# Kernel optimization log

Hardware: AMD Instinct MI355X
Metric: run time of the kernel (lower is better)

Reference implementation:

```python
import jax, jax.numpy as jnp
import numpy as np

B, C, N, T = 8, 128, 512, 64


def setup_inputs() -> dict:
    key = jax.random.key(0)
    ks = jax.random.split(key, 16)
    s = 0.05  # small init scale to keep softmax well-conditioned
    return {
        "x": jax.random.normal(ks[0], (B, C, N, T), jnp.float32),
        "W_w": jax.random.normal(ks[1], (C, C), jnp.float32) * s,
        "W_b": jax.random.normal(ks[2], (C,), jnp.float32) * s,
        "conv_w": jax.random.normal(ks[3], (C, C), jnp.float32) * s,
        "conv_b": jax.random.normal(ks[4], (C,), jnp.float32) * s,
        "theta": jax.random.normal(ks[5], (C, C), jnp.float32) * s,
        "memory": jax.random.normal(ks[6], (N, C), jnp.float32) * s,
        "a_vec": jax.random.uniform(ks[7], (2 * C, 1), jnp.float32) * s,
        "cw": jax.random.normal(ks[8], (N, N), jnp.float32) * s,
        "cwa": jax.random.normal(ks[9], (N, N), jnp.float32) * s,
        "fc_w": jax.random.normal(ks[10], (1, 2), jnp.float32) * s,
        "fc_b": jax.random.normal(ks[11], (1,), jnp.float32) * s,
        "emb": jax.random.normal(ks[12], (1, C, N, 1), jnp.float32),
        "cheb": jax.random.normal(ks[13], (1, N, N), jnp.float32),  # loaded but unused, as in torch forward
    }


def reference(x, W_w, W_b, conv_w, conv_b, theta, memory, a_vec, cw, cwa, fc_w, fc_b, emb, cheb):
    c = x.shape[1]
    skip = x
    # 1x1 conv W: [B,C,N,T] -> [B,C,N,T]
    xw = jnp.einsum('bcnt,dc->bdnt', x, W_w) + W_b[None, :, None, None]
    # Adaptive_Spectral_Block (dropout = identity in eval)
    x_in = jnp.transpose(xw, (0, 3, 2, 1))          # [B,T,N,C]
    h = x_in.sum(axis=1)                             # [B,N,C]
    Wh1 = h @ a_vec[:c]                              # [B,N,1]
    Wh2 = h @ a_vec[c:]                              # [B,N,1]
    e = Wh1 + jnp.transpose(Wh2, (0, 2, 1))          # [B,N,N]
    adj_w = e * cw
    scale = 1.0 / jnp.sqrt(jnp.asarray(c, x.dtype))
    adj1 = jax.nn.softmax(jax.nn.relu(jnp.einsum('btnc,mc->bnm', x_in, memory) * scale), axis=-1)
    adj2 = jax.nn.softmax(jax.nn.relu(jnp.einsum('bnc,bmc->bnm', h, h) * scale), axis=-1)
    # fc: Linear(2,1) over stacked adjacencies, then squeeze
    adj_f = jnp.stack([adj1, adj2], axis=-1) @ fc_w[0] + fc_b[0]   # [B,N,N]
    adj_w = adj_w + adj_f * cwa
    adj_w = jax.nn.softmax(adj_w, axis=-1)
    # top-k (k = int(0.8*N)) + scatter mask
    n = adj_w.shape[-1]
    k = int(n * 0.8)
    _, idx = jax.lax.top_k(adj_w, k)                 # [B,N,k]
    bi = jnp.arange(adj_w.shape[0])[:, None, None]
    ni = jnp.arange(n)[None, :, None]
    mask = jnp.zeros_like(adj_w).at[bi, ni, idx].set(1.0)
    adj = adj_w * mask
    # diffusion aggregation + per-channel Theta transform (single head)
    xh = jnp.einsum('bcnt,bnm->bcmt', xw, adj)
    xh = jnp.einsum('bcnt,cd->bdnt', xh, theta)
    # 1x1 conv over concatenated heads (head=1)
    out = jnp.einsum('bcnt,dc->bdnt', xh, conv_w) + conv_b[None, :, None, None]
    return out * emb + skip
```

## Files before the change

### kernel.cpp

```cpp
#include <hip/hip_runtime.h>
#include <cstdint>
#include <cstddef>

#define KSEL 409u
typedef unsigned short ushort;
typedef short s16x8 __attribute__((ext_vector_type(8)));
typedef float f32x4 __attribute__((ext_vector_type(4)));

union FragU { uint4 u; s16x8 v; };

__device__ __forceinline__ ushort f2bf(float f) {
  union { float f; unsigned u; } x; x.f = f;
  unsigned u = x.u;
  return (ushort)((u + 0x7fffu + ((u >> 16) & 1u)) >> 16);
}

#define OFF_YW     0u
#define OFF_XS     16777216u
#define OFF_H      17301504u
#define OFF_HT     17825792u
#define OFF_WH1    18350080u
#define OFF_WH2    18354176u
#define OFF_ADJ    18358272u
#define OFF_ADJT   20455424u
#define OFF_MEMT   21504000u
#define OFF_WWT    21569536u
#define OFF_M      21585920u
#define OFF_PB16   21602304u
#define OFF_PBIAS  21610496u

__global__ __launch_bounds__(256) void k_pre1(
    const float* __restrict__ memory, const float* __restrict__ W_w,
    const float* __restrict__ conv_w, const float* __restrict__ theta,
    float* __restrict__ memT, float* __restrict__ WwT, float* __restrict__ Mm) {
  int idx = blockIdx.x * 256 + threadIdx.x;
  if (idx < 65536) {
    int c = idx >> 9, m = idx & 511;
    memT[idx] = memory[m * 128 + c];
  } else if (idx < 81920) {
    int i2 = idx - 65536;
    int cp = i2 >> 7, c = i2 & 127;
    WwT[i2] = W_w[c * 128 + cp];
  } else if (idx < 98304) {
    int i3 = idx - 81920;
    int d = i3 >> 7, e = i3 & 127;
    float s = 0.f;
    for (int c = 0; c < 128; ++c) s += conv_w[d * 128 + c] * theta[e * 128 + c];
    Mm[i3] = s;
  }
}

__global__ __launch_bounds__(256) void k_pre2(
    const float* __restrict__ Mm, const float* __restrict__ W_w,
    const float* __restrict__ W_b, ushort* __restrict__ Pb, float* __restrict__ pbias) {
  int idx = blockIdx.x * 256 + threadIdx.x;
  if (idx < 16384) {
    int d = idx >> 7, c = idx & 127;
    float s = 0.f;
    for (int e = 0; e < 128; ++e) s += Mm[d * 128 + e] * W_w[e * 128 + c];
    Pb[d * 128 + c] = f2bf(s);
    if (idx < 128) {
      float s2 = 0.f;
      for (int e = 0; e < 128; ++e) s2 += Mm[idx * 128 + e] * W_b[e];
      pbias[idx] = s2;
    }
  }
}

#define XB_STRIDE 138
#define PB_STRIDE 136
#define OUT_STRIDE 68
__global__ __launch_bounds__(256, 4) void k_yw(
    const float* __restrict__ x, const ushort* __restrict__ Pbg,
    const float* __restrict__ pbias, ushort* __restrict__ ywg, float* __restrict__ Xs) {
  __shared__ __align__(16) ushort pbl[128 * PB_STRIDE];
  __shared__ __align__(16) ushort xbuf[64 * XB_STRIDE];
  __shared__ float pbias_sh[128];
  int bid = blockIdx.x;
  int b = bid >> 9, n = bid & 511;
  int tid = threadIdx.x;
  int lane = tid & 63, w = tid >> 6;
  int quad = lane >> 4, lx = lane & 15;

  for (int k = 0; k < 8; ++k) {
    int flat8 = tid + 256 * k;
    int d = flat8 >> 4, cseg = flat8 & 15;
    uint4 v = *(const uint4*)(Pbg + d * 128 + cseg * 8);
    *(uint4*)&pbl[d * PB_STRIDE + cseg * 8] = v;
  }
  if (tid < 128) pbias_sh[tid] = pbias[tid];

  const float* xbase = x + (size_t)b * 4194304 + (size_t)n * 64;
  for (int k = 0; k < 8; ++k) {
    int c = (tid >> 4) + 16 * k;
    int t0 = (tid & 15) * 4;
    float4 v = *(const float4*)(xbase + (size_t)c * 32768 + t0);
    xbuf[(t0 + 0) * XB_STRIDE + c] = f2bf(v.x);
    xbuf[(t0 + 1) * XB_STRIDE + c] = f2bf(v.y);
    xbuf[(t0 + 2) * XB_STRIDE + c] = f2bf(v.z);
    xbuf[(t0 + 3) * XB_STRIDE + c] = f2bf(v.w);
    float s = v.x + v.y + v.z + v.w;
    s += __shfl_xor(s, 1, 64);
    s += __shfl_xor(s, 2, 64);
    s += __shfl_xor(s, 4, 64);
    s += __shfl_xor(s, 8, 64);
    if ((tid & 15) == 0) Xs[((size_t)(b * 512 + n)) * 128 + c] = s;
  }
  __syncthreads();

  f32x4 acc[8];
  #pragma unroll
  for (int i = 0; i < 8; ++i) acc[i] = (f32x4){0.f, 0.f, 0.f, 0.f};
  int tp = lx + 16 * w;
  const unsigned* xb32 = (const unsigned*)xbuf;
  #pragma unroll
  for (int kc = 0; kc < 4; ++kc) {
    FragU bf;
    int bbase = tp * (XB_STRIDE / 2) + kc * 16 + quad * 4;
    bf.u.x = xb32[bbase + 0];
    bf.u.y = xb32[bbase + 1];
    bf.u.z = xb32[bbase + 2];
    bf.u.w = xb32[bbase + 3];
    #pragma unroll
    for (int dt = 0; dt < 8; ++dt) {
      FragU af;
      af.u = *(const uint4*)&pbl[(16 * dt + lx) * PB_STRIDE + kc * 32 + quad * 8];
      acc[dt] = __builtin_amdgcn_mfma_f32_16x16x32_bf16(af.v, bf.v, acc[dt], 0, 0, 0);
    }
  }
  __syncthreads();
  #pragma unroll
  for (int dt = 0; dt < 8; ++dt)
    #pragma unroll
    for (int r = 0; r < 4; ++r) {
      int d = 16 * dt + quad * 4 + r;
      xbuf[d * OUT_STRIDE + tp] = f2bf(acc[dt][r] + pbias_sh[d]);
    }
  __syncthreads();
  for (int k = 0; k < 4; ++k) {
    int flat8 = tid + 256 * k;
    int d = flat8 >> 3, t0 = (flat8 & 7) * 8;
    ushort4 u0 = *(const ushort4*)&xbuf[d * OUT_STRIDE + t0];
    ushort4 u1 = *(const ushort4*)&xbuf[d * OUT_STRIDE + t0 + 4];
    ushort* dst = ywg + (((size_t)(b * 128 + d)) * 512 + n) * 64 + t0;
    uint4 pk;
    pk.x = (unsigned)u0.x | ((unsigned)u0.y << 16);
    pk.y = (unsigned)u0.z | ((unsigned)u0.w << 16);
    pk.z = (unsigned)u1.x | ((unsigned)u1.y << 16);
    pk.w = (unsigned)u1.z | ((unsigned)u1.w << 16);
    *(uint4*)dst = pk;
  }
}

__global__ __launch_bounds__(256) void k_h(
    const float* __restrict__ Xs, const float* __restrict__ WwT,
    const float* __restrict__ W_b, const float* __restrict__ a_vec,
    float* __restrict__ h, float* __restrict__ hT,
    float* __restrict__ Wh1, float* __restrict__ Wh2) {
  __shared__ float wt[64 * 128];
  __shared__ float xs[8 * 128];
  __shared__ float hr[8 * 128];
  __shared__ float av[256];
  int tid = threadIdx.x;
  int row0 = blockIdx.x * 8;
  for (int i = tid; i < 1024; i += 256) xs[i] = Xs[(size_t)row0 * 128 + i];
  av[tid] = a_vec[tid];
  int c = tid & 127;
  int r0 = tid >> 7;
  float wb = W_b[c] * 64.f;
  float acc[4];
  #pragma unroll
  for (int k = 0; k < 4; ++k) acc[k] = wb;
  for (int ch = 0; ch < 2; ++ch) {
    int cp0 = ch * 64;
    __syncthreads();
    for (int i = tid; i < 8192; i += 256) wt[i] = WwT[(size_t)cp0 * 128 + i];
    __syncthreads();
    for (int cpl = 0; cpl < 64; ++cpl) {
      float w = wt[cpl * 128 + c];
      #pragma unroll
      for (int k = 0; k < 4; ++k) acc[k] += xs[(r0 + 2 * k) * 128 + cp0 + cpl] * w;
    }
  }
  #pragma unroll
  for (int k = 0; k < 4; ++k) {
    int r = r0 + 2 * k;
    int rowg = row0 + r;
    int b = rowg >> 9, n = rowg & 511;
    h[(size_t)rowg * 128 + c] = acc[k];
    hT[((size_t)(b * 128 + c)) * 512 + n] = acc[k];
    hr[r * 128 + c] = acc[k];
  }
  __syncthreads();
  if (tid < 8) {
    float w1 = 0.f, w2 = 0.f;
    for (int cc = 0; cc < 128; ++cc) {
      float hv = hr[tid * 128 + cc];
      w1 += hv * av[cc];
      w2 += hv * av[128 + cc];
    }
    Wh1[row0 + tid] = w1;
    Wh2[row0 + tid] = w2;
  }
}

__device__ __forceinline__ void reduce_rows4(float v[4], float* sred, int tid, bool domax) {
  int lane = tid & 63, wid = tid >> 6;
  #pragma unroll
  for (int off = 32; off > 0; off >>= 1) {
    #pragma unroll
    for (int r = 0; r < 4; ++r) {
      float o = __shfl_down(v[r], off, 64);
      v[r] = domax ? fmaxf(v[r], o) : (v[r] + o);
    }
  }
  if (lane == 0) {
    #pragma unroll
    for (int r = 0; r < 4; ++r) sred[r * 4 + wid] = v[r];
  }
  __syncthreads();
  #pragma unroll
  for (int r = 0; r < 4; ++r) {
    float a0 = sred[r * 4 + 0], a1 = sred[r * 4 + 1];
    float a2 = sred[r * 4 + 2], a3 = sred[r * 4 + 3];
    v[r] = domax ? fmaxf(fmaxf(a0, a1), fmaxf(a2, a3)) : (a0 + a1 + a2 + a3);
  }
  __syncthreads();
}

__device__ __forceinline__ void softmax_rows4(float v[4][2], float* sred, int tid) {
  float mx[4];
  #pragma unroll
  for (int r = 0; r < 4; ++r) mx[r] = fmaxf(v[r][0], v[r][1]);
  reduce_rows4(mx, sred, tid, true);
  float sm[4];
  #pragma unroll
  for (int r = 0; r < 4; ++r) {
    v[r][0] = expf(v[r][0] - mx[r]);
    v[r][1] = expf(v[r][1] - mx[r]);
    sm[r] = v[r][0] + v[r][1];
  }
  reduce_rows4(sm, sred, tid, false);
  #pragma unroll
  for (int r = 0; r < 4; ++r) {
    float inv = 1.f / sm[r];
    v[r][0] *= inv;
    v[r][1] *= inv;
  }
}

__global__ __launch_bounds__(256) void k_adj(
    const float* __restrict__ h, const float* __restrict__ hT,
    const float* __restrict__ memT, const float* __restrict__ Wh1,
    const float* __restrict__ Wh2, const float* __restrict__ cw,
    const float* __restrict__ cwa, const float* __restrict__ fc_w,
    const float* __restrict__ fc_b, float* __restrict__ adj) {
  __shared__ float hn[4 * 128];
  __shared__ float sred[16];
  __shared__ unsigned scnt[124];
  int tid = threadIdx.x;
  int b = blockIdx.x >> 7;
  int n0 = (blockIdx.x & 127) * 4;
  for (int i = tid; i < 512; i += 256) hn[i] = h[((size_t)(b * 512 + n0)) * 128 + i];
  for (int i = tid; i < 124; i += 256) scnt[i] = 0u;
  __syncthreads();
  int m0 = tid, m1 = tid + 256;
  float d1[4][2] = {}, d2[4][2] = {};
  for (int c = 0; c < 128; ++c) {
    float mv0 = memT[c * 512 + m0];
    float mv1 = memT[c * 512 + m1];
    const float* hTr = hT + ((size_t)(b * 128 + c)) * 512;
    float hv0 = hTr[m0];
    float hv1 = hTr[m1];
    #pragma unroll
    for (int r = 0; r < 4; ++r) {
      float hc = hn[r * 128 + c];
      d1[r][0] += hc * mv0; d1[r][1] += hc * mv1;
      d2[r][0] += hc * hv0; d2[r][1] += hc * hv1;
    }
  }
  const float scale = 0.08838834764831845f;
  float l1[4][2], l2[4][2];
  #pragma unroll
  for (int r = 0; r < 4; ++r)
    #pragma unroll
    for (int s = 0; s < 2; ++s) {
      l1[r][s] = fmaxf(d1[r][s] * scale, 0.f);
      l2[r][s] = fmaxf(d2[r][s] * scale, 0.f);
    }
  softmax_rows4(l1, sred, tid);
  softmax_rows4(l2, sred, tid);
  float f0 = fc_w[0], f1 = fc_w[1], fb = fc_b[0];
  float wh2v[2] = {Wh2[b * 512 + m0], Wh2[b * 512 + m1]};
  float aw[4][2];
  #pragma unroll
  for (int r = 0; r < 4; ++r) {
    int n = n0 + r;
    float wh1v = Wh1[b * 512 + n];
    #pragma unroll
    for (int s = 0; s < 2; ++s) {
      int m = s ? m1 : m0;
      float e = wh1v + wh2v[s];
      float adjf = f0 * l1[r][s] + f1 * l2[r][s] + fb;
      aw[r][s] = e * cw[n * 512 + m] + adjf * cwa[n * 512 + m];
    }
  }
  softmax_rows4(aw, sred, tid);
  unsigned ua[4][2];
  #pragma unroll
  for (int r = 0; r < 4; ++r) {
    ua[r][0] = __float_as_uint(aw[r][0]);
    ua[r][1] = __float_as_uint(aw[r][1]);
  }
  unsigned cand[4] = {0u, 0u, 0u, 0u};
  int lane = tid & 63;
  for (int bit = 30; bit >= 0; --bit) {
    unsigned msk = 1u << bit;
    #pragma unroll
    for (int r = 0; r < 4; ++r) {
      unsigned tst = cand[r] | msk;
      unsigned long long b0 = __ballot(ua[r][0] >= tst);
      unsigned long long b1 = __ballot(ua[r][1] >= tst);
      if (lane == 0)
        atomicAdd(&scnt[bit * 4 + r], (unsigned)(__popcll(b0) + __popcll(b1)));
    }
    __syncthreads();
    #pragma unroll
    for (int r = 0; r < 4; ++r)
      if (scnt[bit * 4 + r] >= KSEL) cand[r] |= msk;
  }
  #pragma unroll
  for (int r = 0; r < 4; ++r) {
    size_t base = ((size_t)(b * 512 + n0 + r)) * 512;
    adj[base + m0] = (ua[r][0] >= cand[r]) ? aw[r][0] : 0.f;
    adj[base + m1] = (ua[r][1] >= cand[r]) ? aw[r][1] : 0.f;
  }
}

__global__ __launch_bounds__(256) void k_adjT(
    const float* __restrict__ adj, ushort* __restrict__ adjT) {
  __shared__ float tile[32][33];
  int gid = blockIdx.x;
  int b = gid >> 8;
  int tn = (gid & 255) >> 4, tm = gid & 15;
  int n0 = tn * 32, m0 = tm * 32;
  int tid = threadIdx.x;
  int nl = tid >> 3, ms = (tid & 7) * 4;
  float4 v = *(const float4*)(adj + (size_t)b * 262144 + (size_t)(n0 + nl) * 512 + m0 + ms);
  tile[nl][ms + 0] = v.x; tile[nl][ms + 1] = v.y;
  tile[nl][ms + 2] = v.z; tile[nl][ms + 3] = v.w;
  __syncthreads();
  int ml = tid >> 3, ns = (tid & 7) * 4;
  ushort4 o;
  o.x = f2bf(tile[ns + 0][ml]);
  o.y = f2bf(tile[ns + 1][ml]);
  o.z = f2bf(tile[ns + 2][ml]);
  o.w = f2bf(tile[ns + 3][ml]);
  *(ushort4*)(adjT + (size_t)b * 262144 + (size_t)(m0 + ml) * 512 + n0 + ns) = o;
}

#define AJ_STRIDE 40
#define YB_STRIDE 82
__global__ __launch_bounds__(512, 4) void k_out(
    const ushort* __restrict__ ywg, const ushort* __restrict__ adjT,
    const float* __restrict__ conv_b, const float* __restrict__ emb,
    const float* __restrict__ x, float* __restrict__ out) {
  __shared__ __align__(16) ushort adjt[512 * AJ_STRIDE];
  __shared__ __align__(16) ushort ywb[64 * YB_STRIDE];
  __shared__ float semb[512];
  int gid = blockIdx.x;
  int b = gid >> 7, d = gid & 127;
  int tid = threadIdx.x;
  int lane = tid & 63, w = tid >> 6;
  int quad = lane >> 4, lx = lane & 15;
  for (int i = tid; i < 512; i += 512) semb[i] = emb[d * 512 + i];
  float cb = conv_b[d];
  const ushort* adjTb = adjT + (size_t)b * 262144;
  const ushort* ywbase = ywg + ((size_t)(b * 128 + d)) * 32768;
  f32x4 acc[4][4];
  #pragma unroll
  for (int i = 0; i < 4; ++i)
    #pragma unroll
    for (int j = 0; j < 4; ++j) acc[i][j] = (f32x4){0.f, 0.f, 0.f, 0.f};
  const unsigned* ywb32 = (const unsigned*)ywb;

  for (int nc = 0; nc < 16; ++nc) {
    if (nc) __syncthreads();
    {
      int ml = tid >> 2, seg = tid & 3;
      #pragma unroll
      for (int kk = 0; kk < 4; ++kk) {
        int m = ml + 128 * kk;
        uint4 v = *(const uint4*)(adjTb + (size_t)m * 512 + nc * 32 + seg * 8);
        *(uint4*)&adjt[m * AJ_STRIDE + seg * 8] = v;
      }
    }
    {
      int t = tid & 63, nl = tid >> 6;
      #pragma unroll
      for (int kk = 0; kk < 4; ++kk) {
        int n_loc = nl + 8 * kk;
        ushort v = ywbase[(size_t)(nc * 32 + n_loc) * 64 + t];
        ywb[t * YB_STRIDE + n_loc] = v;
      }
    }
    __syncthreads();
    FragU bf[4];
    #pragma unroll
    for (int tt = 0; tt < 4; ++tt) {
      int t = lx + 16 * tt;
      int bb = t * (YB_STRIDE / 2) + quad * 4;
      bf[tt].u.x = ywb32[bb + 0];
      bf[tt].u.y = ywb32[bb + 1];
      bf[tt].u.z = ywb32[bb + 2];
      bf[tt].u.w = ywb32[bb + 3];
    }
    #pragma unroll
    for (int mt = 0; mt < 4; ++mt) {
      int m = 64 * w + 16 * mt + lx;
      FragU af;
      af.u = *(const uint4*)&adjt[m * AJ_STRIDE + quad * 8];
      #pragma unroll
      for (int tt = 0; tt < 4; ++tt)
        acc[mt][tt] = __builtin_amdgcn_mfma_f32_16x16x32_bf16(af.v, bf[tt].v, acc[mt][tt], 0, 0, 0);
    }
  }
  size_t obase = ((size_t)(b * 128 + d)) * 32768;
  #pragma unroll
  for (int mt = 0; mt < 4; ++mt) {
    #pragma unroll
    for (int r = 0; r < 4; ++r) {
      int m = 64 * w + 16 * mt + quad * 4 + r;
      float em = semb[m];
      #pragma unroll
      for (int tt = 0; tt < 4; ++tt) {
        int t = lx + 16 * tt;
        size_t idx = obase + (size_t)m * 64 + t;
        out[idx] = (acc[mt][tt][r] + cb) * em + x[idx];
      }
    }
  }
}

extern "C" void kernel_launch(void* const* d_in, const int* in_sizes, int n_in,
                              void* d_out, int out_size, void* d_ws, size_t ws_size,
                              hipStream_t stream) {
  const float* x      = (const float*)d_in[0];
  const float* W_w    = (const float*)d_in[1];
  const float* W_b    = (const float*)d_in[2];
  const float* conv_w = (const float*)d_in[3];
  const float* conv_b = (const float*)d_in[4];
  const float* theta  = (const float*)d_in[5];
  const float* memory = (const float*)d_in[6];
  const float* a_vec  = (const float*)d_in[7];
  const float* cw     = (const float*)d_in[8];
  const float* cwa    = (const float*)d_in[9];
  const float* fc_w   = (const float*)d_in[10];
  const float* fc_b   = (const float*)d_in[11];
  const float* emb    = (const float*)d_in[12];
  float* out = (float*)d_out;
  float* ws = (float*)d_ws;
  ushort* ywbf  = (ushort*)(ws + OFF_YW);
  float* Xs     = ws + OFF_XS;
  float* h      = ws + OFF_H;
  float* hT     = ws + OFF_HT;
  float* Wh1    = ws + OFF_WH1;
  float* Wh2    = ws + OFF_WH2;
  float* adj    = ws + OFF_ADJ;
  ushort* adjT  = (ushort*)(ws + OFF_ADJT);
  float* memT   = ws + OFF_MEMT;
  float* WwT    = ws + OFF_WWT;
  float* Mm     = ws + OFF_M;
  ushort* Pb    = (ushort*)(ws + OFF_PB16);
  float* pbias  = ws + OFF_PBIAS;

  hipLaunchKernelGGL(k_pre1, dim3(384), dim3(256), 0, stream,
                     memory, W_w, conv_w, theta, memT, WwT, Mm);
  hipLaunchKernelGGL(k_pre2, dim3(64), dim3(256), 0, stream, Mm, W_w, W_b, Pb, pbias);
  hipLaunchKernelGGL(k_yw, dim3(4096), dim3(256), 0, stream, x, Pb, pbias, ywbf, Xs);
  hipLaunchKernelGGL(k_h, dim3(512), dim3(256), 0, stream,
                     Xs, WwT, W_b, a_vec, h, hT, Wh1, Wh2);
  hipLaunchKernelGGL(k_adj, dim3(1024), dim3(256), 0, stream,
                     h, hT, memT, Wh1, Wh2, cw, cwa, fc_w, fc_b, adj);
  hipLaunchKernelGGL(k_adjT, dim3(2048), dim3(256), 0, stream, adj, adjT);
  hipLaunchKernelGGL(k_out, dim3(1024), dim3(512), 0, stream,
                     ywbf, adjT, conv_b, emb, x, out);
}
```

Measured before the change: 438.0 us.

## Fuse adjacency transpose into k_adj and prefetch k_out tiles into registers

k_adj now writes the masked adjacency directly as transposed bf16, so the fp32 adj buffer and the separate k_adjT transpose kernel are removed. This saves one launch and an fp32 round trip through memory. The cost is scattered 2-byte strided stores from k_adj. Separately, k_out loads the next chunk of adjT and yw into registers while it runs MFMAs on the current chunk, overlapping global latency with compute at the expense of more registers.

Result: no change. 432.0 us (-1.4%).

```diff
diff --git a/kernel.cpp b/kernel.cpp
--- a/kernel.cpp
+++ b/kernel.cpp
@@ -21,13 +21,12 @@
 #define OFF_HT     17825792u
 #define OFF_WH1    18350080u
 #define OFF_WH2    18354176u
-#define OFF_ADJ    18358272u
-#define OFF_ADJT   20455424u
-#define OFF_MEMT   21504000u
-#define OFF_WWT    21569536u
-#define OFF_M      21585920u
-#define OFF_PB16   21602304u
-#define OFF_PBIAS  21610496u
+#define OFF_ADJT   18358272u
+#define OFF_MEMT   19406848u
+#define OFF_WWT    19472384u
+#define OFF_M      19488768u
+#define OFF_PB16   19505152u
+#define OFF_PBIAS  19513344u
 
 __global__ __launch_bounds__(256) void k_pre1(
     const float* __restrict__ memory, const float* __restrict__ W_w,
@@ -254,7 +253,7 @@
     const float* __restrict__ memT, const float* __restrict__ Wh1,
     const float* __restrict__ Wh2, const float* __restrict__ cw,
     const float* __restrict__ cwa, const float* __restrict__ fc_w,
-    const float* __restrict__ fc_b, float* __restrict__ adj) {
+    const float* __restrict__ fc_b, ushort* __restrict__ adjT) {
   __shared__ float hn[4 * 128];
   __shared__ float sred[16];
   __shared__ unsigned scnt[124];
@@ -329,34 +328,13 @@
     for (int r = 0; r < 4; ++r)
       if (scnt[bit * 4 + r] >= KSEL) cand[r] |= msk;
   }
-  #pragma unroll
-  for (int r = 0; r < 4; ++r) {
-    size_t base = ((size_t)(b * 512 + n0 + r)) * 512;
-    adj[base + m0] = (ua[r][0] >= cand[r]) ? aw[r][0] : 0.f;
-    adj[base + m1] = (ua[r][1] >= cand[r]) ? aw[r][1] : 0.f;
-  }
-}
-
-__global__ __launch_bounds__(256) void k_adjT(
-    const float* __restrict__ adj, ushort* __restrict__ adjT) {
-  __shared__ float tile[32][33];
-  int gid = blockIdx.x;
-  int b = gid >> 8;
-  int tn = (gid & 255) >> 4, tm = gid & 15;
-  int n0 = tn * 32, m0 = tm * 32;
-  int tid = threadIdx.x;
-  int nl = tid >> 3, ms = (tid & 7) * 4;
-  float4 v = *(const float4*)(adj + (size_t)b * 262144 + (size_t)(n0 + nl) * 512 + m0 + ms);
-  tile[nl][ms + 0] = v.x; tile[nl][ms + 1] = v.y;
-  tile[nl][ms + 2] = v.z; tile[nl][ms + 3] = v.w;
-  __syncthreads();
-  int ml = tid >> 3, ns = (tid & 7) * 4;
-  ushort4 o;
-  o.x = f2bf(tile[ns + 0][ml]);
-  o.y = f2bf(tile[ns + 1][ml]);
-  o.z = f2bf(tile[ns + 2][ml]);
-  o.w = f2bf(tile[ns + 3][ml]);
-  *(ushort4*)(adjT + (size_t)b * 262144 + (size_t)(m0 + ml) * 512 + n0 + ns) = o;
+  ushort* adjTb = adjT + (size_t)b * 262144;
+  #pragma unroll
+  for (int r = 0; r < 4; ++r) {
+    int n = n0 + r;
+    adjTb[(size_t)m0 * 512 + n] = (ua[r][0] >= cand[r]) ? f2bf(aw[r][0]) : (ushort)0;
+    adjTb[(size_t)m1 * 512 + n] = (ua[r][1] >= cand[r]) ? f2bf(aw[r][1]) : (ushort)0;
+  }
 }
 
 #define AJ_STRIDE 40
@@ -373,7 +351,7 @@
   int tid = threadIdx.x;
   int lane = tid & 63, w = tid >> 6;
   int quad = lane >> 4, lx = lane & 15;
-  for (int i = tid; i < 512; i += 512) semb[i] = emb[d * 512 + i];
+  semb[tid] = emb[d * 512 + tid];
   float cb = conv_b[d];
   const ushort* adjTb = adjT + (size_t)b * 262144;
   const ushort* ywbase = ywg + ((size_t)(b * 128 + d)) * 32768;
@@ -384,27 +362,35 @@
     for (int j = 0; j < 4; ++j) acc[i][j] = (f32x4){0.f, 0.f, 0.f, 0.f};
   const unsigned* ywb32 = (const unsigned*)ywb;
 
+  int aml = tid >> 2, aseg = tid & 3;
+  int yt = tid & 63, ynl = tid >> 6;
+  const ushort* aPtr = adjTb + (size_t)aml * 512 + aseg * 8;
+  uint4 pa0, pa1, pa2, pa3;
+  ushort py0, py1, py2, py3;
+#define LOADC(nc) do {                                               \
+    pa0 = *(const uint4*)(aPtr + (nc) * 32);                         \
+    pa1 = *(const uint4*)(aPtr + 65536 + (nc) * 32);                 \
+    pa2 = *(const uint4*)(aPtr + 131072 + (nc) * 32);                \
+    pa3 = *(const uint4*)(aPtr + 196608 + (nc) * 32);                \
+    py0 = ywbase[(size_t)((nc) * 32 + ynl) * 64 + yt];               \
+    py1 = ywbase[(size_t)((nc) * 32 + ynl + 8) * 64 + yt];           \
+    py2 = ywbase[(size_t)((nc) * 32 + ynl + 16) * 64 + yt];         \
+    py3 = ywbase[(size_t)((nc) * 32 + ynl + 24) * 64 + yt];         \
+  } while (0)
+
+  LOADC(0);
   for (int nc = 0; nc < 16; ++nc) {
-    if (nc) __syncthreads();
-    {
-      int ml = tid >> 2, seg = tid & 3;
-      #pragma unroll
-      for (int kk = 0; kk < 4; ++kk) {
-        int m = ml + 128 * kk;
-        uint4 v = *(const uint4*)(adjTb + (size_t)m * 512 + nc * 32 + seg * 8);
-        *(uint4*)&adjt[m * AJ_STRIDE + seg * 8] = v;
-      }
-    }
-    {
-      int t = tid & 63, nl = tid >> 6;
-      #pragma unroll
-      for (int kk = 0; kk < 4; ++kk) {
-        int n_loc = nl + 8 * kk;
-        ushort v = ywbase[(size_t)(nc * 32 + n_loc) * 64 + t];
-        ywb[t * YB_STRIDE + n_loc] = v;
-      }
-    }
     __syncthreads();
+    *(uint4*)&adjt[(aml      ) * AJ_STRIDE + aseg * 8] = pa0;
+    *(uint4*)&adjt[(aml + 128) * AJ_STRIDE + aseg * 8] = pa1;
+    *(uint4*)&adjt[(aml + 256) * AJ_STRIDE + aseg * 8] = pa2;
+    *(uint4*)&adjt[(aml + 384) * AJ_STRIDE + aseg * 8] = pa3;
+    ywb[yt * YB_STRIDE + ynl     ] = py0;
+    ywb[yt * YB_STRIDE + ynl + 8 ] = py1;
+    ywb[yt * YB_STRIDE + ynl + 16] = py2;
+    ywb[yt * YB_STRIDE + ynl + 24] = py3;
+    __syncthreads();
+    if (nc < 15) LOADC(nc + 1);
     FragU bf[4];
     #pragma unroll
     for (int tt = 0; tt < 4; ++tt) {
@@ -425,6 +411,7 @@
         acc[mt][tt] = __builtin_amdgcn_mfma_f32_16x16x32_bf16(af.v, bf[tt].v, acc[mt][tt], 0, 0, 0);
     }
   }
+#undef LOADC
   size_t obase = ((size_t)(b * 128 + d)) * 32768;
   #pragma unroll
   for (int mt = 0; mt < 4; ++mt) {
@@ -466,7 +453,6 @@
   float* hT     = ws + OFF_HT;
   float* Wh1    = ws + OFF_WH1;
   float* Wh2    = ws + OFF_WH2;
-  float* adj    = ws + OFF_ADJ;
   ushort* adjT  = (ushort*)(ws + OFF_ADJT);
   float* memT   = ws + OFF_MEMT;
   float* WwT    = ws + OFF_WWT;
@@ -481,8 +467,7 @@
   hipLaunchKernelGGL(k_h, dim3(512), dim3(256), 0, stream,
                      Xs, WwT, W_b, a_vec, h, hT, Wh1, Wh2);
   hipLaunchKernelGGL(k_adj, dim3(1024), dim3(256), 0, stream,
-                     h, hT, memT, Wh1, Wh2, cw, cwa, fc_w, fc_b, adj);
-  hipLaunchKernelGGL(k_adjT, dim3(2048), dim3(256), 0, stream, adj, adjT);
+                     h, hT, memT, Wh1, Wh2, cw, cwa, fc_w, fc_b, adjT);
   hipLaunchKernelGGL(k_out, dim3(1024), dim3(512), 0, stream,
                      ywbf, adjT, conv_b, emb, x, out);
 }
```
